# Kernel tuning notes

Measured on AMD Instinct MI355X. Metric: run time of the kernel, lower is better.

The kernel has to match this reference:

```python
import jax, jax.numpy as jnp
import numpy as np

N_NODES = 100000


def sage_conv(x, src, dst, W_l, W_r, b, num_nodes):
    """PyG SAGEConv (aggr='mean', root_weight=True): x@W_l + mean_j(x_j)@W_r + b."""
    msgs = x[src]  # [E, d] irregular gather
    summed = jax.ops.segment_sum(msgs, dst, num_segments=num_nodes)  # [N, d]
    cnt = jax.ops.segment_sum(jnp.ones((src.shape[0],), x.dtype), dst,
                              num_segments=num_nodes)  # [N]
    mean = summed / jnp.maximum(cnt, 1.0)[:, None]
    return x @ W_l + mean @ W_r + b


def setup_inputs() -> dict:
    key = jax.random.key(0)
    ks = jax.random.split(key, 6)
    x = jax.random.normal(ks[0], (N_NODES, 256), dtype=jnp.float32)
    edge_index = jax.random.randint(ks[1], (2, 1600000), 0, N_NODES, dtype=jnp.int32)
    W1_l = jax.random.normal(ks[2], (256, 64), dtype=jnp.float32) * (1.0 / np.sqrt(256))
    W1_r = jax.random.normal(ks[3], (256, 64), dtype=jnp.float32) * (1.0 / np.sqrt(256))
    b1 = jnp.zeros((64,), jnp.float32)
    W2_l = jax.random.normal(ks[4], (64, 40), dtype=jnp.float32) * (1.0 / np.sqrt(64))
    W2_r = jax.random.normal(ks[5], (64, 40), dtype=jnp.float32) * (1.0 / np.sqrt(64))
    b2 = jnp.zeros((40,), jnp.float32)
    return {"x": x, "edge_index": edge_index, "W1_l": W1_l, "W1_r": W1_r,
            "b1": b1, "W2_l": W2_l, "W2_r": W2_r, "b2": b2}


def reference(x, edge_index, W1_l, W1_r, b1, W2_l, W2_r, b2):
    src, dst = edge_index[0], edge_index[1]
    n = x.shape[0]
    h = sage_conv(x, src, dst, W1_l, W1_r, b1, n)
    h = jax.nn.relu(h)
    # F.dropout(training=self.training) -> identity at inference
    h = sage_conv(h, src, dst, W2_l, W2_r, b2, n)
    return jax.nn.softmax(h, axis=1)
```

## Files before the change

### kernel.cpp

```cpp
#include <hip/hip_runtime.h>
#include <hip/hip_bf16.h>
#include <math.h>


typedef __attribute__((ext_vector_type(8))) short bf16x8;
typedef __attribute__((ext_vector_type(4))) float f32x4;

static __device__ __forceinline__ unsigned short f2bf(float f) {
    unsigned int u = __builtin_bit_cast(unsigned int, f);
    unsigned int r = (u + 0x7FFFu + ((u >> 16) & 1u)) >> 16;
    return (unsigned short)r;
}


__global__ void k_count(const int* __restrict__ dst, int* __restrict__ cnt, int E) {
    int e = blockIdx.x * blockDim.x + threadIdx.x;
    if (e < E) atomicAdd(&cnt[dst[e]], 1);
}

__global__ void k_blocksum(const int* __restrict__ cnt, int* __restrict__ bsum, int N) {
    __shared__ int sm[256];
    int i = blockIdx.x * 256 + threadIdx.x;
    sm[threadIdx.x] = (i < N) ? cnt[i] : 0;
    __syncthreads();
    for (int s = 128; s > 0; s >>= 1) {
        if (threadIdx.x < s) sm[threadIdx.x] += sm[threadIdx.x + s];
        __syncthreads();
    }
    if (threadIdx.x == 0) bsum[blockIdx.x] = sm[0];
}

__global__ void k_scanbsum(int* __restrict__ bsum, int nb) {
    __shared__ int a[512], b[512];
    int t = threadIdx.x;
    int v = (t < nb) ? bsum[t] : 0;
    a[t] = v;
    __syncthreads();
    int* pin = a; int* pout = b;
    for (int o = 1; o < 512; o <<= 1) {
        pout[t] = (t >= o) ? pin[t] + pin[t - o] : pin[t];
        __syncthreads();
        int* tmp = pin; pin = pout; pout = tmp;
    }
    if (t < nb) bsum[t] = pin[t] - v;
}

__global__ void k_scanfinal(const int* __restrict__ cnt, const int* __restrict__ bsum,
                            int* __restrict__ off, int* __restrict__ cursor, int N) {
    __shared__ int a[256], b[256];
    int t = threadIdx.x;
    int i = blockIdx.x * 256 + t;
    int v = (i < N) ? cnt[i] : 0;
    a[t] = v;
    __syncthreads();
    int* pin = a; int* pout = b;
    for (int o = 1; o < 256; o <<= 1) {
        pout[t] = (t >= o) ? pin[t] + pin[t - o] : pin[t];
        __syncthreads();
        int* tmp = pin; pin = pout; pout = tmp;
    }
    if (i < N) {
        int ex = bsum[blockIdx.x] + pin[t] - v;
        off[i] = ex;
        cursor[i] = ex;
    }
}

__global__ void k_scatter(const int* __restrict__ src, const int* __restrict__ dst,
                          int* __restrict__ cursor, int* __restrict__ csr, int E) {
    int e = blockIdx.x * blockDim.x + threadIdx.x;
    if (e < E) {
        int d = dst[e];
        int pos = atomicAdd(&cursor[d], 1);
        csr[pos] = src[e];
    }
}


__global__ __launch_bounds__(256) void k_gemm1(const float* __restrict__ x,
                                               const float* __restrict__ Wl,
                                               const float* __restrict__ Wr,
                                               float* __restrict__ y1, int N) {
    __shared__ unsigned short xs[64][40];
    __shared__ unsigned short wsm[128][40];
    int tid = threadIdx.x;
    int row0 = blockIdx.x * 64;
    int lane = tid & 63;
    int wid = tid >> 6;
    int wm = wid >> 1;
    int wn = wid & 1;

    int xr = tid >> 2;
    int xq = tid & 3;
    int wc = tid >> 1;
    int wo = tid & 1;
    const float* wsrc = (wc < 64) ? (Wl + wc) : (Wr + (wc - 64));

    f32x4 acc[2][4];
    #pragma unroll
    for (int m = 0; m < 2; ++m)
        #pragma unroll
        for (int n = 0; n < 4; ++n) acc[m][n] = (f32x4){0.f, 0.f, 0.f, 0.f};

    for (int kk = 0; kk < 256; kk += 32) {
        {
            int grow = row0 + xr;
            float4 v0 = make_float4(0.f, 0.f, 0.f, 0.f);
            float4 v1 = make_float4(0.f, 0.f, 0.f, 0.f);
            if (grow < N) {
                const float* p = x + (size_t)grow * 256 + kk + xq * 8;
                v0 = *(const float4*)(p);
                v1 = *(const float4*)(p + 4);
            }
            bf16x8 pk;
            pk[0] = (short)f2bf(v0.x); pk[1] = (short)f2bf(v0.y);
            pk[2] = (short)f2bf(v0.z); pk[3] = (short)f2bf(v0.w);
            pk[4] = (short)f2bf(v1.x); pk[5] = (short)f2bf(v1.y);
            pk[6] = (short)f2bf(v1.z); pk[7] = (short)f2bf(v1.w);
            *(bf16x8*)(&xs[xr][xq * 8]) = pk;
        }
        {
            bf16x8 w0, w1;
            #pragma unroll
            for (int j = 0; j < 8; ++j)
                w0[j] = (short)f2bf(wsrc[(size_t)(kk + wo * 16 + j) * 64]);
            #pragma unroll
            for (int j = 0; j < 8; ++j)
                w1[j] = (short)f2bf(wsrc[(size_t)(kk + wo * 16 + 8 + j) * 64]);
            *(bf16x8*)(&wsm[wc][wo * 16])     = w0;
            *(bf16x8*)(&wsm[wc][wo * 16 + 8]) = w1;
        }
        __syncthreads();

        int fr = lane & 15;
        int ko = (lane >> 4) * 8;
        bf16x8 a0 = *(const bf16x8*)(&xs[wm * 32 + fr][ko]);
        bf16x8 a1 = *(const bf16x8*)(&xs[wm * 32 + 16 + fr][ko]);
        bf16x8 b0 = *(const bf16x8*)(&wsm[wn * 64 + fr][ko]);
        bf16x8 b1 = *(const bf16x8*)(&wsm[wn * 64 + 16 + fr][ko]);
        bf16x8 b2 = *(const bf16x8*)(&wsm[wn * 64 + 32 + fr][ko]);
        bf16x8 b3 = *(const bf16x8*)(&wsm[wn * 64 + 48 + fr][ko]);

        acc[0][0] = __builtin_amdgcn_mfma_f32_16x16x32_bf16(a0, b0, acc[0][0], 0, 0, 0);
        acc[0][1] = __builtin_amdgcn_mfma_f32_16x16x32_bf16(a0, b1, acc[0][1], 0, 0, 0);
        acc[0][2] = __builtin_amdgcn_mfma_f32_16x16x32_bf16(a0, b2, acc[0][2], 0, 0, 0);
        acc[0][3] = __builtin_amdgcn_mfma_f32_16x16x32_bf16(a0, b3, acc[0][3], 0, 0, 0);
        acc[1][0] = __builtin_amdgcn_mfma_f32_16x16x32_bf16(a1, b0, acc[1][0], 0, 0, 0);
        acc[1][1] = __builtin_amdgcn_mfma_f32_16x16x32_bf16(a1, b1, acc[1][1], 0, 0, 0);
        acc[1][2] = __builtin_amdgcn_mfma_f32_16x16x32_bf16(a1, b2, acc[1][2], 0, 0, 0);
        acc[1][3] = __builtin_amdgcn_mfma_f32_16x16x32_bf16(a1, b3, acc[1][3], 0, 0, 0);
        __syncthreads();
    }

    int cn = lane & 15;
    int r4 = (lane >> 4) * 4;
    #pragma unroll
    for (int m = 0; m < 2; ++m) {
        #pragma unroll
        for (int r = 0; r < 4; ++r) {
            int row = row0 + wm * 32 + m * 16 + r4 + r;
            if (row < N) {
                float* yp = y1 + (size_t)row * 128 + wn * 64 + cn;
                yp[0]  = acc[m][0][r];
                yp[16] = acc[m][1][r];
                yp[32] = acc[m][2][r];
                yp[48] = acc[m][3][r];
            }
        }
    }
}


__global__ __launch_bounds__(256) void k_fused2(const float* __restrict__ y1,
                                                const int* __restrict__ csr,
                                                const int* __restrict__ off,
                                                const int* __restrict__ cnt,
                                                const float* __restrict__ b1,
                                                const float* __restrict__ W2l,
                                                const float* __restrict__ W2r,
                                                float* __restrict__ y2, int N) {
    __shared__ float wsm[64][80];
    __shared__ float hrow[4][64];
    int tid = threadIdx.x;
    #pragma unroll
    for (int it = 0; it < 5; ++it) {
        int idx = tid + it * 256;
        int k = idx / 20;
        int cq = idx % 20;
        const float* s = (cq < 10) ? (W2l + (size_t)k * 40 + cq * 4)
                                   : (W2r + (size_t)k * 40 + (cq - 10) * 4);
        *(float4*)(&wsm[k][cq * 4]) = *(const float4*)s;
    }
    __syncthreads();

    int lane = tid & 63;
    int wv = tid >> 6;
    int wid = blockIdx.x * 4 + wv;
    int nw = gridDim.x * 4;
    float bl = b1[lane];
    int cl = (lane < 40) ? 2 * lane : 0;

    for (int i = wid; i < N; i += nw) {
        int deg = cnt[i];
        int start = off[i];
        float a0 = 0.f, a1 = 0.f, a2 = 0.f, a3 = 0.f;
        for (int base = 0; base < deg; base += 64) {
            int m = min(64, deg - base);
            int s = (lane < m) ? csr[start + base + lane] : 0;
            int j = 0;
            for (; j + 4 <= m; j += 4) {
                int s0 = __shfl(s, j), s1 = __shfl(s, j + 1);
                int s2 = __shfl(s, j + 2), s3 = __shfl(s, j + 3);
                a0 += y1[(size_t)s0 * 128 + 64 + lane];
                a1 += y1[(size_t)s1 * 128 + 64 + lane];
                a2 += y1[(size_t)s2 * 128 + 64 + lane];
                a3 += y1[(size_t)s3 * 128 + 64 + lane];
            }
            for (; j < m; ++j) {
                int sj = __shfl(s, j);
                a0 += y1[(size_t)sj * 128 + 64 + lane];
            }
        }
        float mean = (a0 + a1 + a2 + a3) / (float)max(deg, 1);
        float hv = fmaxf(y1[(size_t)i * 128 + lane] + mean + bl, 0.f);

        hrow[wv][lane] = hv;
        float p0 = 0.f, p1 = 0.f;
        #pragma unroll
        for (int k4 = 0; k4 < 64; k4 += 4) {
            float4 hk = *(const float4*)(&hrow[wv][k4]);
            float2 w0 = *(const float2*)(&wsm[k4 + 0][cl]);
            float2 w1 = *(const float2*)(&wsm[k4 + 1][cl]);
            float2 w2 = *(const float2*)(&wsm[k4 + 2][cl]);
            float2 w3 = *(const float2*)(&wsm[k4 + 3][cl]);
            p0 += hk.x * w0.x + hk.y * w1.x + hk.z * w2.x + hk.w * w3.x;
            p1 += hk.x * w0.y + hk.y * w1.y + hk.z * w2.y + hk.w * w3.y;
        }
        if (lane < 40)
            *(float2*)(y2 + (size_t)i * 80 + cl) = make_float2(p0, p1);
    }
}


__global__ void k_agg2(const float* __restrict__ y2, const int* __restrict__ csr,
                       const int* __restrict__ off, const int* __restrict__ cnt,
                       const float* __restrict__ b2, float* __restrict__ out, int N) {
    int lane = threadIdx.x & 63;
    int wid = (blockIdx.x * blockDim.x + threadIdx.x) >> 6;
    int nw = (gridDim.x * blockDim.x) >> 6;
    for (int i = wid; i < N; i += nw) {
        int deg = cnt[i];
        int start = off[i];
        float a0 = 0.f, a1 = 0.f, a2 = 0.f, a3 = 0.f;
        bool act = (lane < 40);
        for (int base = 0; base < deg; base += 64) {
            int m = min(64, deg - base);
            int s = (lane < m) ? csr[start + base + lane] : 0;
            int j = 0;
            for (; j + 4 <= m; j += 4) {
                int s0 = __shfl(s, j), s1 = __shfl(s, j + 1);
                int s2 = __shfl(s, j + 2), s3 = __shfl(s, j + 3);
                if (act) {
                    a0 += y2[(size_t)s0 * 80 + 40 + lane];
                    a1 += y2[(size_t)s1 * 80 + 40 + lane];
                    a2 += y2[(size_t)s2 * 80 + 40 + lane];
                    a3 += y2[(size_t)s3 * 80 + 40 + lane];
                }
            }
            for (; j < m; ++j) {
                int sj = __shfl(s, j);
                if (act) a0 += y2[(size_t)sj * 80 + 40 + lane];
            }
        }
        float logit = -INFINITY;
        if (act) {
            float mean = (a0 + a1 + a2 + a3) / (float)max(deg, 1);
            logit = y2[(size_t)i * 80 + lane] + mean + b2[lane];
        }
        float mx = logit;
        #pragma unroll
        for (int o = 32; o > 0; o >>= 1) mx = fmaxf(mx, __shfl_xor(mx, o));
        float e = act ? expf(logit - mx) : 0.f;
        float se = e;
        #pragma unroll
        for (int o = 32; o > 0; o >>= 1) se += __shfl_xor(se, o);
        if (act) out[(size_t)i * 40 + lane] = e / se;
    }
}


extern "C" void kernel_launch(void* const* d_in, const int* in_sizes, int n_in,
                              void* d_out, int out_size, void* d_ws, size_t ws_size,
                              hipStream_t stream) {
    const float* x   = (const float*)d_in[0];
    const int*   ei  = (const int*)d_in[1];
    const float* W1l = (const float*)d_in[2];
    const float* W1r = (const float*)d_in[3];
    const float* b1  = (const float*)d_in[4];
    const float* W2l = (const float*)d_in[5];
    const float* W2r = (const float*)d_in[6];
    const float* b2  = (const float*)d_in[7];
    float* out = (float*)d_out;

    int N = in_sizes[0] / 256;
    int E = in_sizes[1] / 2;
    const int* srcp = ei;
    const int* dstp = ei + E;

    char* w = (char*)d_ws;
    auto alloc = [&](size_t bytes) {
        char* p = w;
        w += (bytes + 255) & ~(size_t)255;
        return p;
    };
    int nb = (N + 255) / 256;
    int*   cnt    = (int*)alloc((size_t)N * 4);
    int*   off    = (int*)alloc((size_t)N * 4);
    int*   cursor = (int*)alloc((size_t)N * 4);
    int*   bsum   = (int*)alloc((size_t)nb * 4);
    int*   csr    = (int*)alloc((size_t)E * 4);
    float* y1     = (float*)alloc((size_t)N * 128 * 4);
    float* y2     = (float*)alloc((size_t)N * 80 * 4);

    hipMemsetAsync(cnt, 0, (size_t)N * 4, stream);
    k_count<<<(E + 255) / 256, 256, 0, stream>>>(dstp, cnt, E);
    k_blocksum<<<nb, 256, 0, stream>>>(cnt, bsum, N);
    k_scanbsum<<<1, 512, 0, stream>>>(bsum, nb);
    k_scanfinal<<<nb, 256, 0, stream>>>(cnt, bsum, off, cursor, N);
    k_scatter<<<(E + 255) / 256, 256, 0, stream>>>(srcp, dstp, cursor, csr, E);

    k_gemm1<<<(N + 63) / 64, 256, 0, stream>>>(x, W1l, W1r, y1, N);
    k_fused2<<<1792, 256, 0, stream>>>(y1, csr, off, cnt, b1, W2l, W2r, y2, N);
    k_agg2<<<2048, 256, 0, stream>>>(y2, csr, off, cnt, b2, out, N);
}
```

Measured before the change: 403.2 us.

## Build CSR via two-level bucketed scatter instead of per-node atomic scatter

Replaces the single scatter that did a global atomic per edge on a per-node cursor with a two-pass scheme. The first pass bins each edge into a 128-node bucket using a per-bucket global atomic and writes (src,dst) pairs to a temporary buffer. The second pass has one block per bucket that places the edges into final CSR positions using shared-memory atomics. This is meant to improve write locality of the CSR fill, at the cost of an extra pass, an 8-byte-per-edge temporary buffer, and heavy atomic contention on the much smaller set of bucket counters.

```diff
diff --git a/kernel.cpp b/kernel.cpp
--- a/kernel.cpp
+++ b/kernel.cpp
@@ -46,7 +46,7 @@
 }
 
 __global__ void k_scanfinal(const int* __restrict__ cnt, const int* __restrict__ bsum,
-                            int* __restrict__ off, int* __restrict__ cursor, int N) {
+                            int* __restrict__ off, int* __restrict__ bcur, int N) {
     __shared__ int a[256], b[256];
     int t = threadIdx.x;
     int i = blockIdx.x * 256 + t;
@@ -62,17 +62,39 @@
     if (i < N) {
         int ex = bsum[blockIdx.x] + pin[t] - v;
         off[i] = ex;
-        cursor[i] = ex;
-    }
-}
-
-__global__ void k_scatter(const int* __restrict__ src, const int* __restrict__ dst,
-                          int* __restrict__ cursor, int* __restrict__ csr, int E) {
+        if ((i & 127) == 0) bcur[i >> 7] = ex;
+    }
+}
+
+__global__ void k_binscatter(const int* __restrict__ src, const int* __restrict__ dst,
+                             int* __restrict__ bcur, int2* __restrict__ tmp, int E) {
     int e = blockIdx.x * blockDim.x + threadIdx.x;
     if (e < E) {
         int d = dst[e];
-        int pos = atomicAdd(&cursor[d], 1);
-        csr[pos] = src[e];
+        int pos = atomicAdd(&bcur[d >> 7], 1);
+        tmp[pos] = make_int2(src[e], d);
+    }
+}
+
+__global__ __launch_bounds__(256) void k_bucketscat(const int2* __restrict__ tmp,
+                                                    const int* __restrict__ off,
+                                                    int* __restrict__ csr, int N, int E) {
+    __shared__ int lcur[128];
+    int b = blockIdx.x;
+    int node0 = b << 7;
+    int t = threadIdx.x;
+    if (t < 128) {
+        int node = node0 + t;
+        lcur[t] = (node < N) ? off[node] : 0;
+    }
+    __syncthreads();
+    int start = off[node0];
+    int idx1 = node0 + 128;
+    int end = (idx1 < N) ? off[idx1] : E;
+    for (int e = start + t; e < end; e += 256) {
+        int2 p = tmp[e];
+        int pos = atomicAdd(&lcur[p.y & 127], 1);
+        csr[pos] = p.x;
     }
 }
 
@@ -314,11 +336,13 @@
         return p;
     };
     int nb = (N + 255) / 256;
+    int nbk = (N + 127) >> 7;
     int*   cnt    = (int*)alloc((size_t)N * 4);
     int*   off    = (int*)alloc((size_t)N * 4);
-    int*   cursor = (int*)alloc((size_t)N * 4);
+    int*   bcur   = (int*)alloc((size_t)nbk * 4);
     int*   bsum   = (int*)alloc((size_t)nb * 4);
     int*   csr    = (int*)alloc((size_t)E * 4);
+    int2*  tmp    = (int2*)alloc((size_t)E * 8);
     float* y1     = (float*)alloc((size_t)N * 128 * 4);
     float* y2     = (float*)alloc((size_t)N * 80 * 4);
 
@@ -326,8 +350,9 @@
     k_count<<<(E + 255) / 256, 256, 0, stream>>>(dstp, cnt, E);
     k_blocksum<<<nb, 256, 0, stream>>>(cnt, bsum, N);
     k_scanbsum<<<1, 512, 0, stream>>>(bsum, nb);
-    k_scanfinal<<<nb, 256, 0, stream>>>(cnt, bsum, off, cursor, N);
-    k_scatter<<<(E + 255) / 256, 256, 0, stream>>>(srcp, dstp, cursor, csr, E);
+    k_scanfinal<<<nb, 256, 0, stream>>>(cnt, bsum, off, bcur, N);
+    k_binscatter<<<(E + 255) / 256, 256, 0, stream>>>(srcp, dstp, bcur, tmp, E);
+    k_bucketscat<<<nbk, 256, 0, stream>>>(tmp, off, csr, N, E);
 
     k_gemm1<<<(N + 63) / 64, 256, 0, stream>>>(x, W1l, W1r, y1, N);
     k_fused2<<<1792, 256, 0, stream>>>(y1, csr, off, cnt, b1, W2l, W2r, y2, N);
```

Measured after the change: 666.5 us. +65.3%, slower.
